# Kernel optimization log

Hardware: AMD Instinct MI355X
Metric: run time of the kernel (lower is better)

## Reference

```python
import jax, jax.numpy as jnp
import numpy as np
from jax import lax

B, N, IN, OUT, RANK, P = 8, 7057, 1024, 1024, 64, 84
ALPHA = 1
SCALING = ALPHA / RANK
RATES = (2, 1, 4)


def _cubic(t):
    # PyTorch bicubic kernel (a = -0.75)
    a = -0.75
    at = jnp.abs(t)
    w1 = ((a + 2.0) * at - (a + 3.0)) * at * at + 1.0
    w2 = (((at - 5.0) * at + 8.0) * at - 4.0) * a
    return jnp.where(at <= 1.0, w1, jnp.where(at < 2.0, w2, 0.0))


def _resize_axis(x, out_size, axis):
    # 1-D bicubic resize along `axis`, align_corners=False, border replicate
    in_size = x.shape[axis]
    scale = in_size / out_size
    src = (jnp.arange(out_size, dtype=jnp.float32) + 0.5) * scale - 0.5
    i0 = jnp.floor(src)
    offs = jnp.arange(-1, 3, dtype=jnp.float32)[:, None]  # [4,1]
    pos = i0[None, :] + offs                              # [4,out]
    w = _cubic(src[None, :] - pos)                        # [4,out]
    idx = jnp.clip(pos.astype(jnp.int32), 0, in_size - 1)
    g = jnp.take(x, idx, axis=axis)  # axis -> (4, out)
    wshape = [1] * g.ndim
    wshape[axis] = 4
    wshape[axis + 1] = out_size
    return jnp.sum(g * w.reshape(wshape), axis=axis)


def _bicubic(x, h, w):
    # x: [B,C,H,W] -> [B,C,h,w]
    x = _resize_axis(x, h, axis=2)
    return _resize_axis(x, w, axis=3)


def _expert(x, cw, cb, rate):
    # x: [B,C,H,W]; cw: [C,C,3,3]; cb: [C]
    b, c, h, w = x.shape
    y = _bicubic(x, h * rate, w * rate)
    y = lax.conv_general_dilated(y, cw, (1, 1), [(1, 1), (1, 1)],
                                 dimension_numbers=('NCHW', 'OIHW', 'NCHW'))
    y = y + cb[None, :, None, None]
    y = _bicubic(y, h, w)
    return y.transpose(0, 2, 3, 1).reshape(b, h * w, c)  # [B,HW,C]


def setup_inputs() -> dict:
    key = jax.random.key(0)
    ks = jax.random.split(key, 9)
    return {
        'x': jax.random.normal(ks[0], (B, N, IN), dtype=jnp.float32),
        'W0': jax.random.normal(ks[1], (OUT, IN), dtype=jnp.float32) * 0.02,
        'b0': jax.random.normal(ks[2], (OUT,), dtype=jnp.float32) * 0.02,
        'W_down': jax.random.normal(ks[3], (RANK, IN), dtype=jnp.float32) * 0.02,
        'W_gate': jax.random.uniform(ks[4], (3, RANK), dtype=jnp.float32),
        'b_gate': jax.random.normal(ks[5], (3,), dtype=jnp.float32) * 0.02,
        'conv_w': jax.random.normal(ks[6], (3, RANK, RANK, 3, 3), dtype=jnp.float32) * 0.05,
        'conv_b': jax.random.normal(ks[7], (3, RANK), dtype=jnp.float32) * 0.02,
        'W_up': jax.random.normal(ks[8], (OUT, RANK), dtype=jnp.float32) * 0.02,
    }


def reference(x, W0, b0, W_down, W_gate, b_gate, conv_w, conv_b, W_up):
    out = jnp.einsum('bni,oi->bno', x, W0) + b0            # original layer
    z = jnp.einsum('bni,ri->bnr', x, W_down)               # lora_down (dropout p=0)
    cls_embed = z[:, :1]                                    # [B,1,R]
    feat = z[:, 1:].reshape(B, P, P, RANK).transpose(0, 3, 1, 2)  # [B,R,P,P]
    pooled = feat.mean(axis=(2, 3))                         # AdaptiveAvgPool2d(1)
    gate_score = pooled @ W_gate.T + b_gate                 # [B,3]
    gate_idx = jnp.argmax(gate_score, axis=-1)              # [B]
    eouts = jnp.stack([_expert(feat, conv_w[i], conv_b[i], RATES[i])
                       for i in range(3)], axis=0)          # [3,B,HW,R]
    sel = eouts[gate_idx, jnp.arange(B)] * SCALING          # [B,HW,R]
    lora = jnp.concatenate([cls_embed, sel], axis=1)        # [B,N,R]
    lora_out = jnp.einsum('bnr,or->bno', lora, W_up)
    return out + lora_out
```

## Files before the change

kernel.cpp:

```cpp
#include <hip/hip_runtime.h>
#include <stdint.h>

typedef unsigned short u16;
typedef __bf16 bf16x8 __attribute__((ext_vector_type(8)));
typedef float f32x4 __attribute__((ext_vector_type(4)));

#define B_ 8
#define N_ 7057
#define MTOT 56456
#define SCALING_F (1.0f/64.0f)

#define Z_OFF    0ull
#define LORA_OFF 14452736ull
#define GIDX_OFF 21679104ull
#define CWT_OFF  21679360ull
#define W0B_OFF  21900544ull
#define WDB_OFF  23997696ull
#define WUB_OFF  24128768ull
#define UP_OFF   24259840ull
#define CO_OFF   139865344ull
#define XB_OFF   255470848ull
#define WS_FAST  371092736ull
#define UPB_STRIDE ((size_t)112896 * 64)

__device__ __forceinline__ u16 f2b(float f) {
  __bf16 h = (__bf16)f;
  union { __bf16 h; u16 u; } v; v.h = h; return v.u;
}
__device__ __forceinline__ float b2f(u16 u) {
  union { uint32_t i; float f; } v; v.i = ((uint32_t)u) << 16; return v.f;
}
__device__ __forceinline__ void gload_lds16(const void* g, void* l) {
  __builtin_amdgcn_global_load_lds(
      (const __attribute__((address_space(1))) uint32_t*)g,
      (__attribute__((address_space(3))) uint32_t*)l, 16, 0, 0);
}
__device__ __forceinline__ f32x4 mfma16(bf16x8 a, bf16x8 b, f32x4 c) {
  return __builtin_amdgcn_mfma_f32_16x16x32_bf16(a, b, c, 0, 0, 0);
}
__device__ __forceinline__ bf16x8 cvt8(float4 a, float4 b) {
  bf16x8 v;
  v[0] = (__bf16)a.x; v[1] = (__bf16)a.y; v[2] = (__bf16)a.z; v[3] = (__bf16)a.w;
  v[4] = (__bf16)b.x; v[5] = (__bf16)b.y; v[6] = (__bf16)b.z; v[7] = (__bf16)b.w;
  return v;
}
__device__ __forceinline__ float cubicw(float t) {
  const float a = -0.75f;
  float at = fabsf(t);
  float w1 = ((a + 2.0f) * at - (a + 3.0f)) * at * at + 1.0f;
  float w2 = (((at - 5.0f) * at + 8.0f) * at - 4.0f) * a;
  return at <= 1.0f ? w1 : (at < 2.0f ? w2 : 0.0f);
}
__device__ __forceinline__ int iclamp(int v, int lo, int hi) { return v < lo ? lo : (v > hi ? hi : v); }
__device__ __forceinline__ int rate_of(int e) { return e == 0 ? 2 : (e == 1 ? 1 : 4); }

__global__ __launch_bounds__(256) void cvtall_kernel(const float* __restrict__ W0, const float* __restrict__ Wd,
                                                     const float* __restrict__ Wup, u16* __restrict__ dst) {
  int i = (blockIdx.x * 256 + threadIdx.x) * 4;
  if (i >= 1179648) return;
  const float* src;
  if (i < 1048576)      src = W0 + i;
  else if (i < 1114112) src = Wd + (i - 1048576);
  else                  src = Wup + (i - 1114112);
  float4 v = *(const float4*)src;
  union { u16 u[4]; uint2 q; } p;
  p.u[0] = f2b(v.x); p.u[1] = f2b(v.y); p.u[2] = f2b(v.z); p.u[3] = f2b(v.w);
  *(uint2*)(dst + i) = p.q;
}

__global__ __launch_bounds__(256) void cvtx_kernel(const float* __restrict__ x, u16* __restrict__ xb) {
  size_t stride = (size_t)gridDim.x * 256 * 8;
  for (size_t i = ((size_t)blockIdx.x * 256 + threadIdx.x) * 8; i < (size_t)MTOT * 1024; i += stride) {
    float4 a = *(const float4*)(x + i);
    float4 b = *(const float4*)(x + i + 4);
    *(bf16x8*)(xb + i) = cvt8(a, b);
  }
}

__global__ __launch_bounds__(256) void zgemm_kernel(const float* __restrict__ x,
                                                    const u16* __restrict__ Wdb,
                                                    float* __restrict__ z,
                                                    u16* __restrict__ xb) {
  __shared__ u16 As[64 * 32];
  __shared__ u16 Bs[64 * 32];
  const int tid = threadIdx.x;
  const int lane = tid & 63;
  const int w = tid >> 6;
  const int row0 = blockIdx.x * 64;
  f32x4 acc[4] = {{0,0,0,0},{0,0,0,0},{0,0,0,0},{0,0,0,0}};
  const int srow = tid >> 2, sk8 = tid & 3;
  int arow = row0 + srow; if (arow >= MTOT) arow = MTOT - 1;
  const float* agf = x + (size_t)arow * 1024 + sk8 * 8;
  const u16* bg = Wdb + (size_t)srow * 1024 + sk8 * 8;
  u16* xbp = xb ? (xb + (size_t)arow * 1024 + sk8 * 8) : nullptr;
  u16* al = As + tid * 8;
  u16* bl = Bs + tid * 8;
  const int klo = (lane >> 4) * 8;
  for (int k0 = 0; k0 < 1024; k0 += 32) {
    gload_lds16(bg + k0, bl);
    float4 q0 = *(const float4*)(agf + k0);
    float4 q1 = *(const float4*)(agf + k0 + 4);
    bf16x8 cv = cvt8(q0, q1);
    *(bf16x8*)al = cv;
    if (xbp) *(bf16x8*)(xbp + k0) = cv;
    __syncthreads();
    bf16x8 a = *(const bf16x8*)(As + (w * 16 + (lane & 15)) * 32 + klo);
#pragma unroll
    for (int fc = 0; fc < 4; ++fc) {
      bf16x8 bb = *(const bf16x8*)(Bs + (fc * 16 + (lane & 15)) * 32 + klo);
      acc[fc] = mfma16(a, bb, acc[fc]);
    }
    __syncthreads();
  }
  const int crow = (lane >> 4) * 4, ccol = lane & 15;
#pragma unroll
  for (int fc = 0; fc < 4; ++fc) {
#pragma unroll
    for (int i = 0; i < 4; ++i) {
      int gr = row0 + w * 16 + crow + i;
      if (gr < MTOT) z[(size_t)gr * 64 + fc * 16 + ccol] = acc[fc][i];
    }
  }
}

__global__ __launch_bounds__(256) void convwt_kernel(const float* __restrict__ cw, u16* __restrict__ cwt) {
  int idx = blockIdx.x * 256 + threadIdx.x;
  if (idx >= 3 * 9 * 64 * 64) return;
  int ci = idx & 63;
  int co = (idx >> 6) & 63;
  int rest = idx >> 12;
  int tap = rest % 9;
  int e = rest / 9;
  int sw = ((((ci >> 3) ^ (co & 7)) << 3) | (ci & 7));
  cwt[(((size_t)rest * 64) + co) * 64 + sw] = f2b(cw[((size_t)(e * 64 + co) * 64 + ci) * 9 + tap]);
}

__global__ __launch_bounds__(256) void gate1_kernel(const float* __restrict__ z, float* __restrict__ pp) {
  int b = blockIdx.y, q = blockIdx.x;
  int tid = threadIdx.x;
  int c = tid & 63, part = tid >> 6;
  const float* zb = z + (size_t)b * N_ * 64;
  int n0 = 1 + q * 126;
  float s = 0.0f;
  for (int n = n0 + part; n < n0 + 126; n += 4) s += zb[(size_t)n * 64 + c];
  __shared__ float red[4][64];
  red[part][c] = s;
  __syncthreads();
  if (tid < 64)
    pp[((size_t)b * 56 + q) * 64 + tid] = red[0][tid] + red[1][tid] + red[2][tid] + red[3][tid];
}

__global__ __launch_bounds__(64) void gate2_kernel(const float* __restrict__ pp, const float* __restrict__ z,
                                                   const float* __restrict__ Wg, const float* __restrict__ bg,
                                                   int* __restrict__ gidx, u16* __restrict__ lora) {
  int b = blockIdx.x;
  int c = threadIdx.x;
  float s = 0.0f;
  for (int q = 0; q < 56; ++q) s += pp[((size_t)b * 56 + q) * 64 + c];
  __shared__ float pl[64];
  pl[c] = s * (1.0f / 7056.0f);
  const float* zb = z + (size_t)b * N_ * 64;
  lora[(size_t)b * N_ * 64 + c] = f2b(zb[c]);
  __syncthreads();
  if (c == 0) {
    float best = 0.0f; int bi = 0;
    for (int e = 0; e < 3; ++e) {
      float sc = bg[e];
      for (int r = 0; r < 64; ++r) sc += pl[r] * Wg[e * 64 + r];
      if (e == 0 || sc > best) { best = sc; bi = e; }
    }
    gidx[b] = bi;
  }
}

__global__ __launch_bounds__(256) void conv_kernel(const float* __restrict__ z, const u16* __restrict__ cwt,
                                                   const float* __restrict__ cb, const int* __restrict__ gidx,
                                                   u16* __restrict__ cvo) {
  int b = blockIdx.z;
  int e = gidx[b];
  int r = rate_of(e);
  int H = 84 * r;
  int tx = blockIdx.x, ty = blockIdx.y;
  if (tx * 8 >= H || ty * 8 >= H) return;
  __shared__ __align__(16) float patch[8 * 8 * 64];
  __shared__ u16 halo[100 * 64];
  __shared__ u16 Bw[2][4096];
  __shared__ float hw[100][8];
  __shared__ int hidx[100][8];
  int tid = threadIdx.x, lane = tid & 63, w = tid >> 6;
  const float* zb = z + ((size_t)b * N_ + 1) * 64;
  const u16* wte = cwt + (size_t)e * 9 * 4096;
  gload_lds16(wte + tid * 8, Bw[0] + tid * 8);
  gload_lds16(wte + 2048 + tid * 8, Bw[0] + 2048 + tid * 8);
  if (r == 1) {
    for (int li = tid; li < 800; li += 256) {
      int pix = li >> 3, cq = li & 7;
      int hy = pix / 10, hx = pix - hy * 10;
      int iy = ty * 8 - 1 + hy, ix = tx * 8 - 1 + hx;
      bf16x8 o;
#pragma unroll
      for (int t = 0; t < 8; ++t) o[t] = (__bf16)0.0f;
      if (iy >= 0 && iy < 84 && ix >= 0 && ix < 84) {
        const float* zp = zb + ((size_t)iy * 84 + ix) * 64 + cq * 8;
        float4 q0 = *(const float4*)zp;
        float4 q1 = *(const float4*)(zp + 4);
        o = cvt8(q0, q1);
      }
      *(bf16x8*)(halo + pix * 64 + ((cq ^ (pix & 7)) << 3)) = o;
    }
    __syncthreads();
  } else {
    const int P = (r == 2) ? 8 : 6;
    float inv = 1.0f / (float)r;
    int by = (int)floorf((ty * 8 - 0.5f) * inv - 0.5f) - 1;
    int bx = (int)floorf((tx * 8 - 0.5f) * inv - 0.5f) - 1;
    for (int li = tid; li < P * P * 16; li += 256) {
      int pp_ = li >> 4, f4 = li & 15;
      int py = pp_ / P, px = pp_ - py * P;
      int zr = iclamp(by + py, 0, 83), zc = iclamp(bx + px, 0, 83);
      gload_lds16(zb + ((size_t)zr * 84 + zc) * 64 + f4 * 4, patch + (size_t)li * 4);
    }
    if (tid < 100) {
      int hy = tid / 10, hx = tid - hy * 10;
      int iy = ty * 8 - 1 + hy, ix = tx * 8 - 1 + hx;
      float sy = (iy + 0.5f) * inv - 0.5f;
      float fy = floorf(sy);
      int iy0 = (int)fy;
      float sx = (ix + 0.5f) * inv - 0.5f;
      float fx = floorf(sx);
      int ix0 = (int)fx;
#pragma unroll
      for (int u = 0; u < 4; ++u) {
        hw[tid][u] = cubicw(sy - (fy - 1.0f + u));
        hidx[tid][u] = (iclamp(iy0 - 1 + u, 0, 83) - by) * (P * 64);
        hw[tid][4 + u] = cubicw(sx - (fx - 1.0f + u));
        hidx[tid][4 + u] = (iclamp(ix0 - 1 + u, 0, 83) - bx) * 64;
      }
    }
    __syncthreads();
    for (int li = tid; li < 800; li += 256) {
      int pix = li >> 3, cq = li & 7;
      int hy = pix / 10, hx = pix - hy * 10;
      int iy = ty * 8 - 1 + hy, ix = tx * 8 - 1 + hx;
      bf16x8 o;
#pragma unroll
      for (int t = 0; t < 8; ++t) o[t] = (__bf16)0.0f;
      if (iy >= 0 && iy < H && ix >= 0 && ix < H) {
        float a8[8] = {0.f,0.f,0.f,0.f,0.f,0.f,0.f,0.f};
#pragma unroll
        for (int u = 0; u < 4; ++u) {
          const float* prow = patch + hidx[pix][u] + cq * 8;
          float wyu = hw[pix][u];
#pragma unroll
          for (int v = 0; v < 4; ++v) {
            float wuv = wyu * hw[pix][4 + v];
            const float* pz = prow + hidx[pix][4 + v];
            float4 q0 = *(const float4*)pz;
            float4 q1 = *(const float4*)(pz + 4);
            a8[0] += wuv * q0.x; a8[1] += wuv * q0.y; a8[2] += wuv * q0.z; a8[3] += wuv * q0.w;
            a8[4] += wuv * q1.x; a8[5] += wuv * q1.y; a8[6] += wuv * q1.z; a8[7] += wuv * q1.w;
          }
        }
#pragma unroll
        for (int t = 0; t < 8; ++t) o[t] = (__bf16)a8[t];
      }
      *(bf16x8*)(halo + pix * 64 + ((cq ^ (pix & 7)) << 3)) = o;
    }
    __syncthreads();
  }
  f32x4 acc[4] = {{0,0,0,0},{0,0,0,0},{0,0,0,0},{0,0,0,0}};
  int p = w * 16 + (lane & 15);
  int py = p >> 3, px = p & 7;
  int kg = lane >> 4;
  for (int tap = 0; tap < 9; ++tap) {
    if (tap < 8) {
      const u16* wt = wte + (size_t)(tap + 1) * 4096;
      gload_lds16(wt + tid * 8, Bw[(tap + 1) & 1] + tid * 8);
      gload_lds16(wt + 2048 + tid * 8, Bw[(tap + 1) & 1] + 2048 + tid * 8);
    }
    int dy = tap / 3, dx = tap - dy * 3;
    int pr = (py + dy) * 10 + (px + dx);
    const u16* bwc = Bw[tap & 1];
#pragma unroll
    for (int kk = 0; kk < 2; ++kk) {
      int ch = kk * 4 + kg;
      bf16x8 a = *(const bf16x8*)(halo + pr * 64 + ((ch ^ (pr & 7)) << 3));
#pragma unroll
      for (int fc = 0; fc < 4; ++fc) {
        int co = fc * 16 + (lane & 15);
        bf16x8 bb = *(const bf16x8*)(bwc + co * 64 + ((ch ^ (co & 7)) << 3));
        acc[fc] = mfma16(a, bb, acc[fc]);
      }
    }
    __syncthreads();
  }
  int crow = (lane >> 4) * 4, ccol = lane & 15;
  u16* cvb = cvo + (size_t)b * UPB_STRIDE;
#pragma unroll
  for (int fc = 0; fc < 4; ++fc) {
    int co = fc * 16 + ccol;
    float bias = cb[e * 64 + co];
#pragma unroll
    for (int i = 0; i < 4; ++i) {
      int pd = w * 16 + crow + i;
      int gy = ty * 8 + (pd >> 3), gx = tx * 8 + (pd & 7);
      if (gy < H && gx < H)
        cvb[((size_t)gy * H + gx) * 64 + co] = f2b(acc[fc][i] + bias);
    }
  }
}

__global__ __launch_bounds__(256) void down_kernel(const u16* __restrict__ cvo, const int* __restrict__ gidx,
                                                   u16* __restrict__ lora) {
  int b = blockIdx.z;
  int r = rate_of(gidx[b]);
  int H = 84 * r;
  int tid = threadIdx.x;
  int c = tid & 63, s = tid >> 6;
  int y = blockIdx.y;
  int x = blockIdx.x * 4 + s;
  float fr = (float)r;
  float sy = (y + 0.5f) * fr - 0.5f;
  float fy = floorf(sy);
  int iy0 = (int)fy;
  float wy[4]; int yi[4];
#pragma unroll
  for (int u = 0; u < 4; ++u) { wy[u] = cubicw(sy - (fy - 1.0f + u)); yi[u] = iclamp(iy0 - 1 + u, 0, H - 1); }
  float sx = (x + 0.5f) * fr - 0.5f;
  float fx = floorf(sx);
  int ix0 = (int)fx;
  float wx[4]; int xi[4];
#pragma unroll
  for (int v = 0; v < 4; ++v) { wx[v] = cubicw(sx - (fx - 1.0f + v)); xi[v] = iclamp(ix0 - 1 + v, 0, H - 1); }
  const u16* cbase = cvo + (size_t)b * UPB_STRIDE;
  float acc = 0.0f;
#pragma unroll
  for (int u = 0; u < 4; ++u)
#pragma unroll
    for (int v = 0; v < 4; ++v)
      acc += wy[u] * wx[v] * b2f(cbase[((size_t)yi[u] * H + xi[v]) * 64 + c]);
  lora[((size_t)b * N_ + 1 + y * 84 + x) * 64 + c] = f2b(acc * SCALING_F);
}

__global__ __launch_bounds__(256) void main_gemm(const u16* __restrict__ xb, const u16* __restrict__ W0b,
                                                 const float* __restrict__ b0, const u16* __restrict__ lora,
                                                 const u16* __restrict__ Wub, float* __restrict__ out) {
  __shared__ u16 As[128 * 64];
  __shared__ u16 Bs[128 * 64];
  int tid = threadIdx.x, lane = tid & 63, w = tid >> 6;
  int bid = blockIdx.x;
  int wg = (bid & 7) * 442 + (bid >> 3);
  int row0 = (wg >> 3) * 128, col0 = (wg & 7) * 128;
  int wr = w >> 1, wc = w & 1;
  f32x4 acc[4][4] = {};
  int srow = tid >> 3;
  int schunk = tid & 7;
  int sch8 = ((schunk ^ (srow & 7)) << 3);
  int ar[4]; int br[4];
  u16* aldst[4]; u16* bldst[4];
#pragma unroll
  for (int p = 0; p < 4; ++p) {
    int rr = row0 + p * 32 + srow;
    ar[p] = rr >= MTOT ? MTOT - 1 : rr;
    br[p] = col0 + p * 32 + srow;
    aldst[p] = As + (p * 32 + srow) * 64 + schunk * 8;
    bldst[p] = Bs + (p * 32 + srow) * 64 + schunk * 8;
  }
  for (int k0 = 0; k0 < 1024; k0 += 64) {
#pragma unroll
    for (int p = 0; p < 4; ++p)
      gload_lds16(xb + (size_t)ar[p] * 1024 + k0 + sch8, aldst[p]);
#pragma unroll
    for (int p = 0; p < 4; ++p)
      gload_lds16(W0b + (size_t)br[p] * 1024 + k0 + sch8, bldst[p]);
    __syncthreads();
#pragma unroll
    for (int kk = 0; kk < 2; ++kk) {
      int pc = (((kk << 2) + (lane >> 4)) ^ (lane & 7)) << 3;
      bf16x8 af[4], bfr[4];
#pragma unroll
      for (int fm = 0; fm < 4; ++fm)
        af[fm] = *(const bf16x8*)(As + (wr * 64 + fm * 16 + (lane & 15)) * 64 + pc);
#pragma unroll
      for (int fc = 0; fc < 4; ++fc)
        bfr[fc] = *(const bf16x8*)(Bs + (wc * 64 + fc * 16 + (lane & 15)) * 64 + pc);
#pragma unroll
      for (int fm = 0; fm < 4; ++fm)
#pragma unroll
        for (int fc = 0; fc < 4; ++fc)
          acc[fm][fc] = mfma16(af[fm], bfr[fc], acc[fm][fc]);
    }
    __syncthreads();
  }
#pragma unroll
  for (int p = 0; p < 4; ++p)
    gload_lds16(lora + (size_t)ar[p] * 64 + sch8, aldst[p]);
#pragma unroll
  for (int p = 0; p < 4; ++p)
    gload_lds16(Wub + (size_t)br[p] * 64 + sch8, bldst[p]);
  __syncthreads();
#pragma unroll
  for (int kk = 0; kk < 2; ++kk) {
    int pc = (((kk << 2) + (lane >> 4)) ^ (lane & 7)) << 3;
    bf16x8 af[4], bfr[4];
#pragma unroll
    for (int fm = 0; fm < 4; ++fm)
      af[fm] = *(const bf16x8*)(As + (wr * 64 + fm * 16 + (lane & 15)) * 64 + pc);
#pragma unroll
    for (int fc = 0; fc < 4; ++fc)
      bfr[fc] = *(const bf16x8*)(Bs + (wc * 64 + fc * 16 + (lane & 15)) * 64 + pc);
#pragma unroll
    for (int fm = 0; fm < 4; ++fm)
#pragma unroll
      for (int fc = 0; fc < 4; ++fc)
        acc[fm][fc] = mfma16(af[fm], bfr[fc], acc[fm][fc]);
  }
  __syncthreads();
  int crow = (lane >> 4) * 4, ccol = lane & 15;
#pragma unroll
  for (int fm = 0; fm < 4; ++fm) {
    int grb = row0 + wr * 64 + fm * 16 + crow;
#pragma unroll
    for (int fc = 0; fc < 4; ++fc) {
      int gc = col0 + wc * 64 + fc * 16 + ccol;
      float bias = b0[gc];
#pragma unroll
      for (int i = 0; i < 4; ++i) {
        int gr = grb + i;
        if (gr < MTOT) out[(size_t)gr * 1024 + gc] = acc[fm][fc][i] + bias;
      }
    }
  }
}

extern "C" void kernel_launch(void* const* d_in, const int* in_sizes, int n_in,
                              void* d_out, int out_size, void* d_ws, size_t ws_size,
                              hipStream_t stream) {
  const float* x   = (const float*)d_in[0];
  const float* W0  = (const float*)d_in[1];
  const float* b0  = (const float*)d_in[2];
  const float* Wd  = (const float*)d_in[3];
  const float* Wg  = (const float*)d_in[4];
  const float* bg  = (const float*)d_in[5];
  const float* cw  = (const float*)d_in[6];
  const float* cb  = (const float*)d_in[7];
  const float* Wup = (const float*)d_in[8];
  char* ws = (char*)d_ws;
  float* z    = (float*)(ws + Z_OFF);
  u16* lora   = (u16*)(ws + LORA_OFF);
  int* gidx   = (int*)(ws + GIDX_OFF);
  u16* cwt    = (u16*)(ws + CWT_OFF);
  u16* W0b    = (u16*)(ws + W0B_OFF);
  u16* Wdb    = (u16*)(ws + WDB_OFF);
  u16* Wub    = (u16*)(ws + WUB_OFF);
  float* pp   = (float*)(ws + UP_OFF);
  u16* cvo    = (u16*)(ws + CO_OFF);
  float* out  = (float*)d_out;

  const bool fast = ws_size >= WS_FAST;
  u16* xb = fast ? (u16*)(ws + XB_OFF) : (u16*)(ws + CO_OFF);

  cvtall_kernel<<<dim3(1152), dim3(256), 0, stream>>>(W0, Wd, Wup, W0b);
  convwt_kernel<<<dim3(432), dim3(256), 0, stream>>>(cw, cwt);
  zgemm_kernel<<<dim3(883), dim3(256), 0, stream>>>(x, Wdb, z, fast ? xb : nullptr);
  gate1_kernel<<<dim3(56, 8), dim3(256), 0, stream>>>(z, pp);
  gate2_kernel<<<dim3(8), dim3(64), 0, stream>>>(pp, z, Wg, bg, gidx, lora);
  conv_kernel<<<dim3(42, 42, 8), dim3(256), 0, stream>>>(z, cwt, cb, gidx, cvo);
  down_kernel<<<dim3(21, 84, 8), dim3(256), 0, stream>>>(cvo, gidx, lora);
  if (!fast)
    cvtx_kernel<<<dim3(2048), dim3(256), 0, stream>>>(x, xb);
  main_gemm<<<dim3(3536), dim3(256), 0, stream>>>(xb, W0b, b0, lora, Wub, out);
}
```

Measured before the change: 520.2 us.

## Rewrite main GEMM with 256x256 tiles, double-buffered LDS and explicit waitcnt pipelining

The main bf16 GEMM moves from 128x128 tiles with 256 threads to 256x256 tiles with 512 threads (8 waves). Shared memory is now double-buffered, and loads for the next K step are interleaved with the MFMA phases using explicit vmcnt waits, sched barriers and setprio. The aim is to hide global-to-LDS latency behind compute and to raise operand reuse per tile. The cost is 128KB of LDS, more accumulator registers and fewer blocks (884) for the XCD-remapped grid, which raises occupancy and tail-imbalance risks.

Result: no change. 520.4 us (+0.0%).

```diff
diff --git a/kernel.cpp b/kernel.cpp
--- a/kernel.cpp
+++ b/kernel.cpp
@@ -22,6 +22,10 @@
 #define XB_OFF   255470848ull
 #define WS_FAST  371092736ull
 #define UPB_STRIDE ((size_t)112896 * 64)
+
+#define SBAR() { __builtin_amdgcn_sched_barrier(0); __builtin_amdgcn_s_barrier(); __builtin_amdgcn_sched_barrier(0); }
+#define VMW2() { asm volatile("s_waitcnt vmcnt(2)" ::: "memory"); __builtin_amdgcn_sched_barrier(0); }
+#define VMW0() { asm volatile("s_waitcnt vmcnt(0)" ::: "memory"); __builtin_amdgcn_sched_barrier(0); }
 
 __device__ __forceinline__ u16 f2b(float f) {
   __bf16 h = (__bf16)f;
@@ -342,92 +346,134 @@
   lora[((size_t)b * N_ + 1 + y * 84 + x) * 64 + c] = f2b(acc * SCALING_F);
 }
 
-__global__ __launch_bounds__(256) void main_gemm(const u16* __restrict__ xb, const u16* __restrict__ W0b,
-                                                 const float* __restrict__ b0, const u16* __restrict__ lora,
-                                                 const u16* __restrict__ Wub, float* __restrict__ out) {
-  __shared__ u16 As[128 * 64];
-  __shared__ u16 Bs[128 * 64];
+__global__ __launch_bounds__(512, 2) void main_gemm(const u16* __restrict__ xb, const u16* __restrict__ W0b,
+                                                    const float* __restrict__ b0, const u16* __restrict__ lora,
+                                                    const u16* __restrict__ Wub, float* __restrict__ out) {
+  __shared__ u16 As[2][256 * 64];
+  __shared__ u16 Bs[2][256 * 64];
   int tid = threadIdx.x, lane = tid & 63, w = tid >> 6;
   int bid = blockIdx.x;
-  int wg = (bid & 7) * 442 + (bid >> 3);
-  int row0 = (wg >> 3) * 128, col0 = (wg & 7) * 128;
-  int wr = w >> 1, wc = w & 1;
-  f32x4 acc[4][4] = {};
-  int srow = tid >> 3;
-  int schunk = tid & 7;
-  int sch8 = ((schunk ^ (srow & 7)) << 3);
-  int ar[4]; int br[4];
-  u16* aldst[4]; u16* bldst[4];
-#pragma unroll
-  for (int p = 0; p < 4; ++p) {
-    int rr = row0 + p * 32 + srow;
-    ar[p] = rr >= MTOT ? MTOT - 1 : rr;
-    br[p] = col0 + p * 32 + srow;
-    aldst[p] = As + (p * 32 + srow) * 64 + schunk * 8;
-    bldst[p] = Bs + (p * 32 + srow) * 64 + schunk * 8;
-  }
-  for (int k0 = 0; k0 < 1024; k0 += 64) {
-#pragma unroll
-    for (int p = 0; p < 4; ++p)
-      gload_lds16(xb + (size_t)ar[p] * 1024 + k0 + sch8, aldst[p]);
-#pragma unroll
-    for (int p = 0; p < 4; ++p)
-      gload_lds16(W0b + (size_t)br[p] * 1024 + k0 + sch8, bldst[p]);
-    __syncthreads();
-#pragma unroll
-    for (int kk = 0; kk < 2; ++kk) {
-      int pc = (((kk << 2) + (lane >> 4)) ^ (lane & 7)) << 3;
-      bf16x8 af[4], bfr[4];
-#pragma unroll
-      for (int fm = 0; fm < 4; ++fm)
-        af[fm] = *(const bf16x8*)(As + (wr * 64 + fm * 16 + (lane & 15)) * 64 + pc);
-#pragma unroll
-      for (int fc = 0; fc < 4; ++fc)
-        bfr[fc] = *(const bf16x8*)(Bs + (wc * 64 + fc * 16 + (lane & 15)) * 64 + pc);
-#pragma unroll
-      for (int fm = 0; fm < 4; ++fm)
-#pragma unroll
-        for (int fc = 0; fc < 4; ++fc)
-          acc[fm][fc] = mfma16(af[fm], bfr[fc], acc[fm][fc]);
-    }
-    __syncthreads();
-  }
-#pragma unroll
-  for (int p = 0; p < 4; ++p)
-    gload_lds16(lora + (size_t)ar[p] * 64 + sch8, aldst[p]);
-#pragma unroll
-  for (int p = 0; p < 4; ++p)
-    gload_lds16(Wub + (size_t)br[p] * 64 + sch8, bldst[p]);
+  int xcd = bid & 7, loc = bid >> 3;
+  int wg = (xcd < 4 ? xcd * 111 : 444 + (xcd - 4) * 110) + loc;
+  int row0 = (wg >> 2) * 256, col0 = (wg & 3) * 256;
+  int wr = w >> 2, wc = w & 3;
+  int srow_[2], swk_[2], dof_[2], arow_[2][2];
+#pragma unroll
+  for (int j = 0; j < 2; ++j) {
+    int slot = w * 2 + j;
+    int srow = slot * 8 + (lane >> 3);
+    int chunk = lane & 7;
+    srow_[j] = srow;
+    swk_[j] = ((chunk ^ (srow & 7)) << 3);
+    dof_[j] = srow * 64 + chunk * 8;
+#pragma unroll
+    for (int h = 0; h < 2; ++h) {
+      int rr = row0 + h * 128 + srow;
+      arow_[h][j] = rr >= MTOT ? MTOT - 1 : rr;
+    }
+  }
+  auto stageA = [&](int buf, int h, int k0) {
+#pragma unroll
+    for (int j = 0; j < 2; ++j)
+      gload_lds16(xb + (size_t)arow_[h][j] * 1024 + k0 + swk_[j], &As[buf][h * 8192 + dof_[j]]);
+  };
+  auto stageB = [&](int buf, int h, int k0) {
+#pragma unroll
+    for (int j = 0; j < 2; ++j)
+      gload_lds16(W0b + (size_t)(col0 + h * 128 + srow_[j]) * 1024 + k0 + swk_[j], &Bs[buf][h * 8192 + dof_[j]]);
+  };
+  f32x4 acc[8][4] = {};
+  int l15 = lane & 15;
+  int pc0 = ((lane >> 4) ^ (lane & 7)) << 3;
+  int pc1 = ((4 + (lane >> 4)) ^ (lane & 7)) << 3;
+  stageA(0, 0, 0); stageA(0, 1, 0); stageB(0, 0, 0); stageB(0, 1, 0);
+  stageA(1, 0, 64);
+  for (int t = 0; t < 16; ++t) {
+    int cur = t & 1, oth = cur ^ 1;
+    int k1 = (t + 1) << 6;
+    if (t < 15) { VMW2(); } else { VMW0(); }
+    SBAR();
+    const u16* Ac = As[cur];
+    const u16* Bc = Bs[cur];
+    bf16x8 bfr[4][2];
+#pragma unroll
+    for (int n = 0; n < 4; ++n) {
+      int cb = (wc * 64 + n * 16 + l15) * 64;
+      bfr[n][0] = *(const bf16x8*)(Bc + cb + pc0);
+      bfr[n][1] = *(const bf16x8*)(Bc + cb + pc1);
+    }
+#pragma unroll
+    for (int ph = 0; ph < 4; ++ph) {
+      bf16x8 a[2][2];
+#pragma unroll
+      for (int m2 = 0; m2 < 2; ++m2) {
+        int ca = (wr * 128 + (ph * 2 + m2) * 16 + l15) * 64;
+        a[m2][0] = *(const bf16x8*)(Ac + ca + pc0);
+        a[m2][1] = *(const bf16x8*)(Ac + ca + pc1);
+      }
+      if (t < 15) {
+        if (ph == 0) stageA(oth, 1, k1);
+        else if (ph == 1) stageB(oth, 0, k1);
+        else if (ph == 2) stageB(oth, 1, k1);
+      }
+      __builtin_amdgcn_s_setprio(1);
+#pragma unroll
+      for (int m2 = 0; m2 < 2; ++m2) {
+        int mf = ph * 2 + m2;
+#pragma unroll
+        for (int n = 0; n < 4; ++n) {
+          acc[mf][n] = mfma16(a[m2][0], bfr[n][0], acc[mf][n]);
+          acc[mf][n] = mfma16(a[m2][1], bfr[n][1], acc[mf][n]);
+        }
+      }
+      __builtin_amdgcn_s_setprio(0);
+    }
+    SBAR();
+    if (t < 14) stageA(cur, 0, (t + 2) << 6);
+  }
   __syncthreads();
 #pragma unroll
-  for (int kk = 0; kk < 2; ++kk) {
-    int pc = (((kk << 2) + (lane >> 4)) ^ (lane & 7)) << 3;
-    bf16x8 af[4], bfr[4];
-#pragma unroll
-    for (int fm = 0; fm < 4; ++fm)
-      af[fm] = *(const bf16x8*)(As + (wr * 64 + fm * 16 + (lane & 15)) * 64 + pc);
-#pragma unroll
-    for (int fc = 0; fc < 4; ++fc)
-      bfr[fc] = *(const bf16x8*)(Bs + (wc * 64 + fc * 16 + (lane & 15)) * 64 + pc);
-#pragma unroll
-    for (int fm = 0; fm < 4; ++fm)
-#pragma unroll
-      for (int fc = 0; fc < 4; ++fc)
-        acc[fm][fc] = mfma16(af[fm], bfr[fc], acc[fm][fc]);
+  for (int j = 0; j < 2; ++j) {
+    gload_lds16(lora + (size_t)arow_[0][j] * 64 + swk_[j], &As[0][dof_[j]]);
+    gload_lds16(lora + (size_t)arow_[1][j] * 64 + swk_[j], &As[0][8192 + dof_[j]]);
+    gload_lds16(Wub + (size_t)(col0 + srow_[j]) * 64 + swk_[j], &Bs[0][dof_[j]]);
+    gload_lds16(Wub + (size_t)(col0 + 128 + srow_[j]) * 64 + swk_[j], &Bs[0][8192 + dof_[j]]);
   }
   __syncthreads();
-  int crow = (lane >> 4) * 4, ccol = lane & 15;
-#pragma unroll
-  for (int fm = 0; fm < 4; ++fm) {
-    int grb = row0 + wr * 64 + fm * 16 + crow;
-#pragma unroll
-    for (int fc = 0; fc < 4; ++fc) {
-      int gc = col0 + wc * 64 + fc * 16 + ccol;
+  {
+    const u16* Ac = As[0];
+    const u16* Bc = Bs[0];
+    bf16x8 bfr[4][2];
+#pragma unroll
+    for (int n = 0; n < 4; ++n) {
+      int cb = (wc * 64 + n * 16 + l15) * 64;
+      bfr[n][0] = *(const bf16x8*)(Bc + cb + pc0);
+      bfr[n][1] = *(const bf16x8*)(Bc + cb + pc1);
+    }
+#pragma unroll
+    for (int mf = 0; mf < 8; ++mf) {
+      int ca = (wr * 128 + mf * 16 + l15) * 64;
+      bf16x8 a0 = *(const bf16x8*)(Ac + ca + pc0);
+      bf16x8 a1 = *(const bf16x8*)(Ac + ca + pc1);
+#pragma unroll
+      for (int n = 0; n < 4; ++n) {
+        acc[mf][n] = mfma16(a0, bfr[n][0], acc[mf][n]);
+        acc[mf][n] = mfma16(a1, bfr[n][1], acc[mf][n]);
+      }
+    }
+  }
+  int crow = (lane >> 4) * 4;
+#pragma unroll
+  for (int mf = 0; mf < 8; ++mf) {
+    int grb = row0 + wr * 128 + mf * 16 + crow;
+#pragma unroll
+    for (int n = 0; n < 4; ++n) {
+      int gc = col0 + wc * 64 + n * 16 + l15;
       float bias = b0[gc];
 #pragma unroll
       for (int i = 0; i < 4; ++i) {
         int gr = grb + i;
-        if (gr < MTOT) out[(size_t)gr * 1024 + gc] = acc[fm][fc][i] + bias;
+        if (gr < MTOT) out[(size_t)gr * 1024 + gc] = acc[mf][n][i] + bias;
       }
     }
   }
@@ -469,5 +515,5 @@
   down_kernel<<<dim3(21, 84, 8), dim3(256), 0, stream>>>(cvo, gidx, lora);
   if (!fast)
     cvtx_kernel<<<dim3(2048), dim3(256), 0, stream>>>(x, xb);
-  main_gemm<<<dim3(3536), dim3(256), 0, stream>>>(xb, W0b, b0, lora, Wub, out);
-}
+  main_gemm<<<dim3(884), dim3(512), 0, stream>>>(xb, W0b, b0, lora, Wub, out);
+}
```

## Double-buffer zgemm LDS tiles and XOR-swizzle conv patch layout

Applied to the files above, without the earlier changes.

The z projection GEMM now uses two LDS buffers, staging the next K slice while MFMAs run on the current one, and drops one barrier per iteration. The conv kernel's bicubic source patch is stored with an XOR swizzle of 32-byte channel chunks keyed on pixel index, and the reads undo it, to cut LDS bank conflicts during upsampling. The cost is double the zgemm LDS, an extra small index table, and more address arithmetic in the inner interpolation loop.

New measurement: 523.0 us. No clear change (+0.5%).

```diff
diff --git a/kernel.cpp b/kernel.cpp
--- a/kernel.cpp
+++ b/kernel.cpp
@@ -81,8 +81,8 @@
                                                     const u16* __restrict__ Wdb,
                                                     float* __restrict__ z,
                                                     u16* __restrict__ xb) {
-  __shared__ u16 As[64 * 32];
-  __shared__ u16 Bs[64 * 32];
+  __shared__ u16 As[2][64 * 32];
+  __shared__ u16 Bs[2][64 * 32];
   const int tid = threadIdx.x;
   const int lane = tid & 63;
   const int w = tid >> 6;
@@ -93,21 +93,24 @@
   const float* agf = x + (size_t)arow * 1024 + sk8 * 8;
   const u16* bg = Wdb + (size_t)srow * 1024 + sk8 * 8;
   u16* xbp = xb ? (xb + (size_t)arow * 1024 + sk8 * 8) : nullptr;
-  u16* al = As + tid * 8;
-  u16* bl = Bs + tid * 8;
   const int klo = (lane >> 4) * 8;
-  for (int k0 = 0; k0 < 1024; k0 += 32) {
-    gload_lds16(bg + k0, bl);
+  auto STG = [&](int b, int k0) {
+    gload_lds16(bg + k0, &Bs[b][tid * 8]);
     float4 q0 = *(const float4*)(agf + k0);
     float4 q1 = *(const float4*)(agf + k0 + 4);
     bf16x8 cv = cvt8(q0, q1);
-    *(bf16x8*)al = cv;
+    *(bf16x8*)&As[b][tid * 8] = cv;
     if (xbp) *(bf16x8*)(xbp + k0) = cv;
-    __syncthreads();
-    bf16x8 a = *(const bf16x8*)(As + (w * 16 + (lane & 15)) * 32 + klo);
+  };
+  STG(0, 0);
+  __syncthreads();
+  for (int k0 = 0; k0 < 1024; k0 += 32) {
+    int cur = (k0 >> 5) & 1;
+    if (k0 < 992) STG(cur ^ 1, k0 + 32);
+    bf16x8 a = *(const bf16x8*)&As[cur][(w * 16 + (lane & 15)) * 32 + klo];
 #pragma unroll
     for (int fc = 0; fc < 4; ++fc) {
-      bf16x8 bb = *(const bf16x8*)(Bs + (fc * 16 + (lane & 15)) * 32 + klo);
+      bf16x8 bb = *(const bf16x8*)&Bs[cur][(fc * 16 + (lane & 15)) * 32 + klo];
       acc[fc] = mfma16(a, bb, acc[fc]);
     }
     __syncthreads();
@@ -187,6 +190,7 @@
   __shared__ u16 Bw[2][4096];
   __shared__ float hw[100][8];
   __shared__ int hidx[100][8];
+  __shared__ u16 hs[100][8];
   int tid = threadIdx.x, lane = tid & 63, w = tid >> 6;
   const float* zb = z + ((size_t)b * N_ + 1) * 64;
   const u16* wte = cwt + (size_t)e * 9 * 4096;
@@ -218,7 +222,8 @@
       int pp_ = li >> 4, f4 = li & 15;
       int py = pp_ / P, px = pp_ - py * P;
       int zr = iclamp(by + py, 0, 83), zc = iclamp(bx + px, 0, 83);
-      gload_lds16(zb + ((size_t)zr * 84 + zc) * 64 + f4 * 4, patch + (size_t)li * 4);
+      int sf4 = (f4 & 1) | ((((f4 >> 1) ^ (pp_ & 7)) & 7) << 1);
+      gload_lds16(zb + ((size_t)zr * 84 + zc) * 64 + sf4 * 4, patch + (size_t)li * 4);
     }
     if (tid < 100) {
       int hy = tid / 10, hx = tid - hy * 10;
@@ -231,10 +236,14 @@
       int ix0 = (int)fx;
 #pragma unroll
       for (int u = 0; u < 4; ++u) {
+        int ry = iclamp(iy0 - 1 + u, 0, 83) - by;
+        int rx = iclamp(ix0 - 1 + u, 0, 83) - bx;
         hw[tid][u] = cubicw(sy - (fy - 1.0f + u));
-        hidx[tid][u] = (iclamp(iy0 - 1 + u, 0, 83) - by) * (P * 64);
+        hidx[tid][u] = ry * (P * 64);
+        hs[tid][u] = (u16)((ry * P) & 7);
         hw[tid][4 + u] = cubicw(sx - (fx - 1.0f + u));
-        hidx[tid][4 + u] = (iclamp(ix0 - 1 + u, 0, 83) - bx) * 64;
+        hidx[tid][4 + u] = rx * 64;
+        hs[tid][4 + u] = (u16)(rx & 7);
       }
     }
     __syncthreads();
@@ -249,12 +258,14 @@
         float a8[8] = {0.f,0.f,0.f,0.f,0.f,0.f,0.f,0.f};
 #pragma unroll
         for (int u = 0; u < 4; ++u) {
-          const float* prow = patch + hidx[pix][u] + cq * 8;
+          const float* prow = patch + hidx[pix][u];
+          int hsy = hs[pix][u];
           float wyu = hw[pix][u];
 #pragma unroll
           for (int v = 0; v < 4; ++v) {
             float wuv = wyu * hw[pix][4 + v];
-            const float* pz = prow + hidx[pix][4 + v];
+            int s = (hsy + hs[pix][4 + v]) & 7;
+            const float* pz = prow + hidx[pix][4 + v] + ((cq ^ s) << 3);
             float4 q0 = *(const float4*)pz;
             float4 q1 = *(const float4*)(pz + 4);
             a8[0] += wuv * q0.x; a8[1] += wuv * q0.y; a8[2] += wuv * q0.z; a8[3] += wuv * q0.w;
```
